# Performance work log

Hardware: AMD Instinct MI355X
Metric: run time of the kernel (lower is better)

## Reference

```python
import jax, jax.numpy as jnp
import numpy as np

B, N, F_IN, F_OUT = 8, 2048, 128, 128


def setup_inputs() -> dict:
    key = jax.random.key(0)
    k1, k2, k3, k4 = jax.random.split(key, 4)
    stdv = 1.0 / np.sqrt(F_OUT)
    X = jax.random.normal(k1, (B, N, F_IN), dtype=jnp.float32)
    adj = jax.random.uniform(k2, (B, N, N), dtype=jnp.float32)
    W = jax.random.uniform(k3, (F_IN, F_OUT), minval=-stdv, maxval=stdv, dtype=jnp.float32)
    b = jax.random.uniform(k4, (F_OUT,), minval=-stdv, maxval=stdv, dtype=jnp.float32)
    return {"X": X, "adj": adj, "W": W, "b": b}


def reference(X, adj, W, b):
    # XW: [B, N, F_out]
    XW = jnp.einsum('bnf,fo->bno', X, W)
    # adj + I (self loops)
    adj = adj + jnp.eye(adj.shape[1], dtype=adj.dtype)[None]
    # symmetric degree normalization: D^-1/2 A D^-1/2, done as row/col scaling
    d = jnp.sum(adj, axis=-1)                 # [B, N]
    r = d ** -0.5                             # [B, N]
    adj = adj * r[:, :, None] * r[:, None, :] # [B, N, N]
    y = jnp.einsum('bnm,bmo->bno', adj, XW) + b
    return jax.nn.leaky_relu(y, negative_slope=0.01)
```

## Files before the change

### kernel.cpp

```cpp
#include <hip/hip_runtime.h>
#include <hip/hip_bf16.h>

#define BB 8
#define NN 2048
#define FD 128

typedef float f32x4 __attribute__((ext_vector_type(4)));
typedef short bf16x8 __attribute__((ext_vector_type(8)));
typedef short s16x4 __attribute__((ext_vector_type(4)));

__device__ __forceinline__ short f2bf(float f) {
  union { __hip_bfloat16 h; short s; } u;
  u.h = __float2bfloat16(f);
  return u.s;
}

__global__ __launch_bounds__(256) void k_degree(const float* __restrict__ adj,
                                                float* __restrict__ r) {
  const int row  = blockIdx.x * 4 + (threadIdx.x >> 6);
  const int lane = threadIdx.x & 63;
  const f32x4* p = reinterpret_cast<const f32x4*>(adj + (size_t)row * NN);
  float s = 0.f;
#pragma unroll
  for (int i = 0; i < 8; ++i) {
    f32x4 v = p[lane + 64 * i];
    s += (v.x + v.y) + (v.z + v.w);
  }
#pragma unroll
  for (int off = 32; off >= 1; off >>= 1) s += __shfl_xor(s, off, 64);
  if (lane == 0) r[row] = rsqrtf(1.0f + s);
}

__global__ __launch_bounds__(256) void k_xw(const float* __restrict__ X,
                                            const float* __restrict__ W,
                                            const float* __restrict__ r,
                                            short* __restrict__ bpack,
                                            float* __restrict__ xwsr) {
  __shared__ __align__(16) float Xs[64][132];
  __shared__ __align__(16) float Ws[128][128];
  const int b  = blockIdx.y;
  const int m0 = blockIdx.x * 64;
  const int t  = threadIdx.x;
  {
    const f32x4* wp = reinterpret_cast<const f32x4*>(W);
    f32x4* wd = reinterpret_cast<f32x4*>(&Ws[0][0]);
#pragma unroll
    for (int i = 0; i < 16; ++i) wd[t + 256 * i] = wp[t + 256 * i];
    const f32x4* xp = reinterpret_cast<const f32x4*>(X + ((size_t)b * NN + m0) * FD);
#pragma unroll
    for (int i = 0; i < 8; ++i) {
      int slot = t + 256 * i;
      f32x4 v = xp[slot];
      *reinterpret_cast<f32x4*>(&Xs[slot >> 5][(slot & 31) * 4]) = v;
    }
  }
  __syncthreads();
  const int ot = (t & 15) * 8;
  const int mt = (t >> 4) * 4;
  float acc[4][8];
#pragma unroll
  for (int i = 0; i < 4; ++i)
#pragma unroll
    for (int j = 0; j < 8; ++j) acc[i][j] = 0.f;

  for (int k = 0; k < 128; k += 4) {
    f32x4 xv[4];
#pragma unroll
    for (int i = 0; i < 4; ++i) xv[i] = *reinterpret_cast<const f32x4*>(&Xs[mt + i][k]);
#pragma unroll
    for (int kk = 0; kk < 4; ++kk) {
      float wv[8];
#pragma unroll
      for (int j = 0; j < 8; ++j) wv[j] = Ws[k + kk][ot + j];
#pragma unroll
      for (int i = 0; i < 4; ++i)
#pragma unroll
        for (int j = 0; j < 8; ++j) acc[i][j] = fmaf(xv[i][kk], wv[j], acc[i][j]);
    }
  }
  const int bm = b * NN + m0 + mt;
#pragma unroll
  for (int i = 0; i < 4; ++i) {
    float rm = r[bm + i];
#pragma unroll
    for (int j = 0; j < 8; ++j) acc[i][j] *= rm;
  }
#pragma unroll
  for (int i = 0; i < 4; ++i) {
    f32x4 lo = {acc[i][0], acc[i][1], acc[i][2], acc[i][3]};
    f32x4 hi = {acc[i][4], acc[i][5], acc[i][6], acc[i][7]};
    float* dst = xwsr + (size_t)(bm + i) * FD + ot;
    *reinterpret_cast<f32x4*>(dst) = lo;
    *reinterpret_cast<f32x4*>(dst + 4) = hi;
  }
  short* bp = bpack + (size_t)b * NN * FD;
  const int grp = (m0 + mt) >> 3;
  const int h   = ((m0 + mt) >> 2) & 1;
#pragma unroll
  for (int j = 0; j < 8; ++j) {
    s16x4 sv;
#pragma unroll
    for (int i = 0; i < 4; ++i) sv[i] = f2bf(acc[i][j]);
    *reinterpret_cast<s16x4*>(bp + (size_t)grp * 1024 + (ot + j) * 8 + h * 4) = sv;
  }
}

#define NT 16
__global__ __launch_bounds__(256, 4) void k_gemm5(const float* __restrict__ adj,
                                                  const short* __restrict__ bpack,
                                                  const float* __restrict__ xwsr,
                                                  const float* __restrict__ r,
                                                  const float* __restrict__ bias,
                                                  float* __restrict__ out) {
  __shared__ __align__(16) short As[2][16 * 128];
  const int b    = blockIdx.y;
  const int n0   = blockIdx.x * 16;
  const int t    = threadIdx.x;
  const int lane = t & 63;
  const int w    = t >> 6;

  const int sr = t >> 4;
  const int su = t & 15;
  const float* gsrc = adj + ((size_t)b * NN + n0 + sr) * NN + su * 8;
  const int wofs = sr * 256 + ((su ^ (sr & 7)) << 4);

  const int fr = lane & 15;
  const int kg = lane >> 4;
  const short* bpb = bpack + (size_t)b * NN * FD + (size_t)kg * 1024 + (w * 32 + fr) * 8;

  f32x4 acc[2];
  acc[0] = (f32x4){0.f, 0.f, 0.f, 0.f};
  acc[1] = (f32x4){0.f, 0.f, 0.f, 0.f};

  f32x4 ga[2];
  bf16x8 Bev[4][2], Bod[4][2];

  auto issueA = [&](int kt) {
    const f32x4* p = reinterpret_cast<const f32x4*>(gsrc + (size_t)kt * 128);
    ga[0] = p[0];
    ga[1] = p[1];
  };
  auto issueB = [&](int kt, bf16x8 (&d)[4][2]) {
    const short* bt = bpb + (size_t)kt * 16 * 1024;
#pragma unroll
    for (int kf = 0; kf < 4; ++kf)
#pragma unroll
      for (int cf = 0; cf < 2; ++cf)
        d[kf][cf] = *reinterpret_cast<const bf16x8*>(bt + (size_t)kf * 4096 + cf * 128);
  };
  auto commitA = [&](int buf) {
    bf16x8 o;
#pragma unroll
    for (int i = 0; i < 4; ++i) { o[i] = f2bf(ga[0][i]); o[4 + i] = f2bf(ga[1][i]); }
    *reinterpret_cast<bf16x8*>(reinterpret_cast<char*>(&As[buf][0]) + wofs) = o;
  };
  auto compute = [&](int buf, bf16x8 (&bs)[4][2]) {
    const char* abase = reinterpret_cast<const char*>(&As[buf][0]);
#pragma unroll
    for (int kf = 0; kf < 4; ++kf) {
      bf16x8 af = *reinterpret_cast<const bf16x8*>(
          abase + fr * 256 + (((kf * 4 + kg) ^ (fr & 7)) << 4));
      acc[0] = __builtin_amdgcn_mfma_f32_16x16x32_bf16(af, bs[kf][0], acc[0], 0, 0, 0);
      acc[1] = __builtin_amdgcn_mfma_f32_16x16x32_bf16(af, bs[kf][1], acc[1], 0, 0, 0);
    }
  };

  issueA(0);
  issueB(0, Bev);
  commitA(0);
  __syncthreads();

#pragma unroll
  for (int kt = 0; kt < NT; ++kt) {
    const int cur = kt & 1;
    if (kt + 1 < NT) issueA(kt + 1);
    if (kt + 1 < NT) {
      if (cur) issueB(kt + 1, Bev); else issueB(kt + 1, Bod);
    }
    if (cur) compute(1, Bod); else compute(0, Bev);
    if (kt + 1 < NT) commitA(cur ^ 1);
    __syncthreads();
  }

  const int col = lane & 15, rq = lane >> 4;
  const float* xr = xwsr + ((size_t)b * NN + n0) * FD;
  float* ob = out + ((size_t)b * NN + n0) * FD;
#pragma unroll
  for (int reg = 0; reg < 4; ++reg) {
    const int rloc = rq * 4 + reg;
    const float rn = r[b * NN + n0 + rloc];
#pragma unroll
    for (int cf = 0; cf < 2; ++cf) {
      const int o = w * 32 + cf * 16 + col;
      float v = acc[cf][reg] + xr[(size_t)rloc * FD + o];
      v = rn * v + bias[o];
      ob[(size_t)rloc * FD + o] = v > 0.f ? v : 0.01f * v;
    }
  }
}

extern "C" void kernel_launch(void* const* d_in, const int* in_sizes, int n_in,
                              void* d_out, int out_size, void* d_ws, size_t ws_size,
                              hipStream_t stream) {
  (void)in_sizes; (void)n_in; (void)out_size; (void)ws_size;
  const float* X    = (const float*)d_in[0];
  const float* adj  = (const float*)d_in[1];
  const float* W    = (const float*)d_in[2];
  const float* bias = (const float*)d_in[3];
  float* out = (float*)d_out;

  char* ws = (char*)d_ws;
  float* r     = (float*)ws;
  short* bpack = (short*)(ws + 65536);
  float* xwsr  = (float*)(ws + 4259840);

  k_degree<<<dim3(BB * NN / 4), dim3(256), 0, stream>>>(adj, r);
  k_xw<<<dim3(NN / 64, BB), dim3(256), 0, stream>>>(X, W, r, bpack, xwsr);
  k_gemm5<<<dim3(NN / 16, BB), dim3(256), 0, stream>>>(adj, bpack, xwsr, r, bias, out);
}
```

Baseline: 73.99 us.

## Deepen adj prefetch to two tiles ahead and use LDS-only barriers in GEMM

The adj-times-XW GEMM now prefetches the fp32 adj tile two k-steps ahead using two register buffers, with the loop unrolled by two so buffers alternate statically. It replaces __syncthreads with an explicit lgkmcnt(0) wait plus s_barrier, fenced by sched_barrier, so outstanding global loads need not drain at each barrier. Launch bounds drop from 4 to 3 waves per SIMD to make room for the extra registers. The aim is to keep more HBM reads in flight to hide latency on the memory-bound adj stream, at the cost of occupancy.

```diff
diff --git a/kernel.cpp b/kernel.cpp
--- a/kernel.cpp
+++ b/kernel.cpp
@@ -106,7 +106,7 @@
 }
 
 #define NT 16
-__global__ __launch_bounds__(256, 4) void k_gemm5(const float* __restrict__ adj,
+__global__ __launch_bounds__(256, 3) void k_gemm6(const float* __restrict__ adj,
                                                   const short* __restrict__ bpack,
                                                   const float* __restrict__ xwsr,
                                                   const float* __restrict__ r,
@@ -132,13 +132,13 @@
   acc[0] = (f32x4){0.f, 0.f, 0.f, 0.f};
   acc[1] = (f32x4){0.f, 0.f, 0.f, 0.f};
 
-  f32x4 ga[2];
-  bf16x8 Bev[4][2], Bod[4][2];
-
-  auto issueA = [&](int kt) {
+  f32x4 ga0[2], ga1[2];
+  bf16x8 B0[4][2], B1[4][2];
+
+  auto issueA = [&](int kt, f32x4 (&d)[2]) {
     const f32x4* p = reinterpret_cast<const f32x4*>(gsrc + (size_t)kt * 128);
-    ga[0] = p[0];
-    ga[1] = p[1];
+    d[0] = p[0];
+    d[1] = p[1];
   };
   auto issueB = [&](int kt, bf16x8 (&d)[4][2]) {
     const short* bt = bpb + (size_t)kt * 16 * 1024;
@@ -148,10 +148,10 @@
       for (int cf = 0; cf < 2; ++cf)
         d[kf][cf] = *reinterpret_cast<const bf16x8*>(bt + (size_t)kf * 4096 + cf * 128);
   };
-  auto commitA = [&](int buf) {
+  auto commitA = [&](int buf, f32x4 (&s)[2]) {
     bf16x8 o;
 #pragma unroll
-    for (int i = 0; i < 4; ++i) { o[i] = f2bf(ga[0][i]); o[4 + i] = f2bf(ga[1][i]); }
+    for (int i = 0; i < 4; ++i) { o[i] = f2bf(s[0][i]); o[4 + i] = f2bf(s[1][i]); }
     *reinterpret_cast<bf16x8*>(reinterpret_cast<char*>(&As[buf][0]) + wofs) = o;
   };
   auto compute = [&](int buf, bf16x8 (&bs)[4][2]) {
@@ -164,22 +164,37 @@
       acc[1] = __builtin_amdgcn_mfma_f32_16x16x32_bf16(af, bs[kf][1], acc[1], 0, 0, 0);
     }
   };
-
-  issueA(0);
-  issueB(0, Bev);
-  commitA(0);
-  __syncthreads();
-
-#pragma unroll
-  for (int kt = 0; kt < NT; ++kt) {
-    const int cur = kt & 1;
-    if (kt + 1 < NT) issueA(kt + 1);
-    if (kt + 1 < NT) {
-      if (cur) issueB(kt + 1, Bev); else issueB(kt + 1, Bod);
-    }
-    if (cur) compute(1, Bod); else compute(0, Bev);
-    if (kt + 1 < NT) commitA(cur ^ 1);
-    __syncthreads();
+  auto barrier_lgkm = [&]() {
+    asm volatile("s_waitcnt lgkmcnt(0)" ::: "memory");
+    __builtin_amdgcn_sched_barrier(0);
+    __builtin_amdgcn_s_barrier();
+    __builtin_amdgcn_sched_barrier(0);
+  };
+
+  issueA(0, ga0);
+  issueB(0, B0);
+  commitA(0, ga0);
+  issueA(1, ga1);
+  barrier_lgkm();
+
+#pragma unroll
+  for (int kt2 = 0; kt2 < NT; kt2 += 2) {
+    {
+      const int kt = kt2;
+      if (kt + 2 < NT) issueA(kt + 2, ga0);
+      if (kt + 1 < NT) issueB(kt + 1, B1);
+      compute(0, B0);
+      if (kt + 1 < NT) commitA(1, ga1);
+      barrier_lgkm();
+    }
+    {
+      const int kt = kt2 + 1;
+      if (kt + 2 < NT) issueA(kt + 2, ga1);
+      if (kt + 1 < NT) issueB(kt + 1, B0);
+      compute(1, B1);
+      if (kt + 1 < NT) commitA(0, ga0);
+      barrier_lgkm();
+    }
   }
 
   const int col = lane & 15, rq = lane >> 4;
@@ -216,5 +231,5 @@
 
   k_degree<<<dim3(BB * NN / 4), dim3(256), 0, stream>>>(adj, r);
   k_xw<<<dim3(NN / 64, BB), dim3(256), 0, stream>>>(X, W, r, bpack, xwsr);
-  k_gemm5<<<dim3(NN / 16, BB), dim3(256), 0, stream>>>(adj, bpack, xwsr, r, bias, out);
-}
+  k_gemm6<<<dim3(NN / 16, BB), dim3(256), 0, stream>>>(adj, bpack, xwsr, r, bias, out);
+}
```

Measured after the change: 74.43 us. No clear change (+0.6%).
